# Optimization experiments

Hardware: AMD Instinct MI355X
Metric: run time of the kernel (lower is better)

The kernel has to match this reference:

```python
import jax, jax.numpy as jnp
import numpy as np
from jax import lax

RES = 64  # feature-map resolution after the stride-2 maxpool (input_size // 2)


def build_grid(res):
    # [1, res, res, 4]: (y, x, 1-y, 1-x) normalized coords, matching torch build_grid
    r = jnp.linspace(0.0, 1.0, res)
    yy, xx = jnp.meshgrid(r, r, indexing='ij')
    g = jnp.stack([yy, xx], axis=-1)[None]  # [1, res, res, 2]
    return jnp.concatenate([g, 1.0 - g], axis=-1)


def setup_inputs() -> dict:
    key = jax.random.key(0)
    ks = jax.random.split(key, 8)
    B, O, S = 8, 32, 128
    images = jax.random.normal(ks[0], (B, 12, S, S), dtype=jnp.float32)
    rois = jax.random.randint(ks[1], (B, O, S, S), 0, 2) > 0  # bool object masks
    gt_pos = jax.random.uniform(ks[2], (B, 4, O, 2), dtype=jnp.float32)
    conv1_w = jax.random.normal(ks[3], (64, 12, 7, 7), dtype=jnp.float32) * 0.05
    conv1_b = jnp.zeros((64,), dtype=jnp.float32)
    conv2_w = jax.random.normal(ks[4], (128, 64, 3, 3), dtype=jnp.float32) * 0.05
    conv2_b = jnp.zeros((128,), dtype=jnp.float32)
    pe_w = jax.random.normal(ks[5], (128, 4), dtype=jnp.float32) * 0.5
    pe_b = jnp.zeros((128,), dtype=jnp.float32)
    return {"images": images, "rois": rois, "gt_pos": gt_pos,
            "conv1_w": conv1_w, "conv1_b": conv1_b,
            "conv2_w": conv2_w, "conv2_b": conv2_b,
            "pe_w": pe_w, "pe_b": pe_b}


def _forward(images, rois, conv1_w, conv1_b, conv2_w, conv2_b, pe_w, pe_b):
    dn = ('NCHW', 'OIHW', 'NCHW')
    # conv1 7x7 pad 3 + ReLU
    x = lax.conv_general_dilated(images, conv1_w, (1, 1), [(3, 3), (3, 3)], dimension_numbers=dn)
    x = jax.nn.relu(x + conv1_b[None, :, None, None])
    # maxpool 2x2 stride 2
    x = lax.reduce_window(x, -jnp.inf, lax.max, (1, 1, 2, 2), (1, 1, 2, 2), 'VALID')
    # conv2 3x3 pad 1 + ReLU -> [B, 128, 64, 64]
    x = lax.conv_general_dilated(x, conv2_w, (1, 1), [(1, 1), (1, 1)], dimension_numbers=dn)
    x = jax.nn.relu(x + conv2_b[None, :, None, None])
    # soft position embedding: Linear(4->128) on grid, added per-pixel
    grid = build_grid(RES)  # [1, 64, 64, 4]
    emb = jnp.einsum('ihwf,cf->ichw', grid, pe_w) + pe_b[None, :, None, None]
    x = x + emb
    # roi_pool: nearest-downsample masks 128->64 (stride-2 gather matches torch nearest),
    # broadcast-multiply, then spatial max -> [B, O, C]
    m = rois[:, :, ::2, ::2].astype(x.dtype)  # [B, O, 64, 64]
    masked = x[:, None] * m[:, :, None]       # [B, O, C, 64, 64] (huge intermediate)
    return jnp.max(masked, axis=(-1, -2))


def reference(images, rois, gt_pos, conv1_w, conv1_b, conv2_w, conv2_b, pe_w, pe_b):
    # gt_pos is unused because use_ground_truth_pos=False
    return _forward(images, rois, conv1_w, conv1_b, conv2_w, conv2_b, pe_w, pe_b)
```

## Files before the change

kernel.cpp:

```cpp
#include <hip/hip_runtime.h>
#include <math.h>

typedef __attribute__((ext_vector_type(8))) short bf16x8;
typedef __attribute__((ext_vector_type(4))) float f32x4;
typedef __attribute__((ext_vector_type(8))) unsigned short ushort8;

#define N_IMT  (8*136*136*16)
#define N_PT   (8*66*66*64)
#define N_X2   (8*128*64*64)
#define N_PARTIAL (8*32*8*128)
#define N_WB1  (25*4*64*8)
#define N_WB2  (18*8*64*8)

__device__ inline unsigned short f2bf(float f) {
    unsigned u = __float_as_uint(f);
    u += 0x7FFF + ((u >> 16) & 1);
    return (unsigned short)(u >> 16);
}
__device__ inline float bf2f(unsigned short h) {
    return __uint_as_float(((unsigned)h) << 16);
}

__global__ void k_zero(unsigned* __restrict__ p, int n) {
    int stride = gridDim.x * 256;
    for (int i = blockIdx.x * 256 + threadIdx.x; i < n; i += stride) p[i] = 0u;
}

__global__ void k_prep(const float* __restrict__ images,
                       const float* __restrict__ w1, const float* __restrict__ w2,
                       unsigned short* __restrict__ imTh, unsigned short* __restrict__ imTl,
                       unsigned short* __restrict__ wB1h, unsigned short* __restrict__ wB1l,
                       unsigned short* __restrict__ wB2h, unsigned short* __restrict__ wB2l)
{
    const int bid = blockIdx.x, tid = threadIdx.x;
    if (bid < 512) {
        int t = bid * 256 + tid;
        int b = t >> 14, rem = t & 16383;
        int y = rem >> 7, x = rem & 127;
        ushort8 h0, h1, l0, l1;
        #pragma unroll
        for (int j = 0; j < 8; ++j) {
            float v = images[((b * 12 + j) << 14) + (y << 7) + x];
            unsigned short h = f2bf(v);
            h0[j] = h; l0[j] = f2bf(v - bf2f(h));
        }
        #pragma unroll
        for (int j = 0; j < 4; ++j) {
            float v = images[((b * 12 + 8 + j) << 14) + (y << 7) + x];
            unsigned short h = f2bf(v);
            h1[j] = h; l1[j] = f2bf(v - bf2f(h));
        }
        #pragma unroll
        for (int j = 4; j < 8; ++j) { h1[j] = 0; l1[j] = 0; }
        int base = ((b * 136 + y + 3) * 136 + x + 3) * 16;
        *(ushort8*)(imTh + base) = h0;  *(ushort8*)(imTh + base + 8) = h1;
        *(ushort8*)(imTl + base) = l0;  *(ushort8*)(imTl + base + 8) = l1;
    } else if (bid < 537) {
        int s = bid - 512;
        int n = tid >> 6, l = tid & 63;
        int oc = n * 16 + (l & 15), g = l >> 4;
        int tap = 2 * s + (g >> 1);
        ushort8 hi, lo;
        #pragma unroll
        for (int j = 0; j < 8; ++j) {
            int ic = (g & 1) * 8 + j;
            float v = (tap < 49 && ic < 12) ? w1[oc * 588 + ic * 49 + tap] : 0.0f;
            unsigned short h = f2bf(v);
            hi[j] = h; lo[j] = f2bf(v - bf2f(h));
        }
        int idx = ((s * 4 + n) * 64 + l) * 8;
        *(ushort8*)(wB1h + idx) = hi;  *(ushort8*)(wB1l + idx) = lo;
    } else {
        int u = bid - 537;
        int s = u >> 1, nh = u & 1;
        int n = nh * 4 + (tid >> 6), l = tid & 63;
        int oc = n * 16 + (l & 15);
        int tap = s >> 1;
        ushort8 hi, lo;
        #pragma unroll
        for (int j = 0; j < 8; ++j) {
            int ic = (s & 1) * 32 + (l >> 4) * 8 + j;
            float v = w2[oc * 576 + ic * 9 + tap];
            unsigned short h = f2bf(v);
            hi[j] = h; lo[j] = f2bf(v - bf2f(h));
        }
        int idx = ((s * 8 + n) * 64 + l) * 8;
        *(ushort8*)(wB2h + idx) = hi;  *(ushort8*)(wB2l + idx) = lo;
    }
}

__global__ __launch_bounds__(256, 4) void k1_mfma(
    const unsigned short* __restrict__ imTh, const unsigned short* __restrict__ imTl,
    const unsigned short* __restrict__ wB1h, const unsigned short* __restrict__ wB1l,
    const float* __restrict__ b1,
    unsigned short* __restrict__ pTh, unsigned short* __restrict__ pTl)
{
    const int bid = blockIdx.x;
    const int b  = bid & 7;
    const int rest = bid >> 3;
    const int y0 = rest & 63;
    const int x0 = (rest >> 6) * 64;
    const int tid = threadIdx.x;
    const int w  = __builtin_amdgcn_readfirstlane(tid >> 6);
    const int l  = tid & 63;
    const int px = l & 15;
    const int g  = l >> 4;
    const int gq = g >> 1;
    const int baseA = ((b * 136 + 2 * y0) * 136 + (x0 + w * 16 + px)) * 16 + (g & 1) * 8;

    f32x4 acc[2][4];
    #pragma unroll
    for (int m = 0; m < 2; ++m)
        #pragma unroll
        for (int n = 0; n < 4; ++n) acc[m][n] = (f32x4)(0.0f);

    #pragma unroll
    for (int s = 0; s < 25; ++s) {
        const int t0 = 2 * s, t1 = 2 * s + 1;
        const int off0 = ((t0 / 7) * 136 + (t0 % 7)) * 16;
        const int off1 = ((t1 / 7) * 136 + (t1 % 7)) * 16;
        int offA = gq ? off1 : off0;
        bf16x8 Ah0 = *(const bf16x8*)(imTh + baseA + offA);
        bf16x8 Ah1 = *(const bf16x8*)(imTh + baseA + 2176 + offA);
        bf16x8 Al0 = *(const bf16x8*)(imTl + baseA + offA);
        bf16x8 Al1 = *(const bf16x8*)(imTl + baseA + 2176 + offA);
        const unsigned short* wb = wB1h + s * 2048 + l * 8;
        const unsigned short* wl2 = wB1l + s * 2048 + l * 8;
        #pragma unroll
        for (int n = 0; n < 4; ++n) {
            bf16x8 Bh = *(const bf16x8*)(wb + n * 512);
            bf16x8 Bl = *(const bf16x8*)(wl2 + n * 512);
            acc[0][n] = __builtin_amdgcn_mfma_f32_16x16x32_bf16(Ah0, Bh, acc[0][n], 0, 0, 0);
            acc[0][n] = __builtin_amdgcn_mfma_f32_16x16x32_bf16(Ah0, Bl, acc[0][n], 0, 0, 0);
            acc[0][n] = __builtin_amdgcn_mfma_f32_16x16x32_bf16(Al0, Bh, acc[0][n], 0, 0, 0);
            acc[1][n] = __builtin_amdgcn_mfma_f32_16x16x32_bf16(Ah1, Bh, acc[1][n], 0, 0, 0);
            acc[1][n] = __builtin_amdgcn_mfma_f32_16x16x32_bf16(Ah1, Bl, acc[1][n], 0, 0, 0);
            acc[1][n] = __builtin_amdgcn_mfma_f32_16x16x32_bf16(Al1, Bh, acc[1][n], 0, 0, 0);
        }
    }

    #pragma unroll
    for (int n = 0; n < 4; ++n) {
        int oc = n * 16 + px;
        float bias = b1[oc];
        #pragma unroll
        for (int pp = 0; pp < 2; ++pp) {
            int e = pp * 2;
            float m = fmaxf(fmaxf(acc[0][n][e], acc[0][n][e + 1]),
                            fmaxf(acc[1][n][e], acc[1][n][e + 1]));
            float v = fmaxf(m + bias, 0.0f);
            unsigned short h = f2bf(v);
            unsigned short lo = f2bf(v - bf2f(h));
            int pcol = (x0 >> 1) + w * 8 + g * 2 + pp;
            int pidx = ((b * 66 + y0 + 1) * 66 + pcol + 1) * 64 + oc;
            pTh[pidx] = h; pTl[pidx] = lo;
        }
    }
}

__global__ __launch_bounds__(256, 4) void k2_mfma(
    const unsigned short* __restrict__ pTh, const unsigned short* __restrict__ pTl,
    const unsigned short* __restrict__ wB2h, const unsigned short* __restrict__ wB2l,
    const float* __restrict__ b2, const float* __restrict__ pew,
    const float* __restrict__ peb, float* __restrict__ x2)
{
    const int bid = blockIdx.x;
    const int b   = bid & 7;
    const int rest = bid >> 3;
    const int y   = rest & 63;
    const int ocg = rest >> 6;
    const int tid = threadIdx.x;
    const int w  = __builtin_amdgcn_readfirstlane(tid >> 6);
    const int l  = tid & 63;
    const int px = l & 15;
    const int g  = l >> 4;
    const int baseA = ((b * 66 + y) * 66 + (w * 16 + px)) * 64 + g * 8;

    f32x4 acc[4];
    #pragma unroll
    for (int n = 0; n < 4; ++n) acc[n] = (f32x4)(0.0f);

    #pragma unroll
    for (int s = 0; s < 18; ++s) {
        const int tap = s >> 1;
        const int offA = ((tap / 3) * 66 + (tap % 3)) * 64 + (s & 1) * 32;
        bf16x8 Ah = *(const bf16x8*)(pTh + baseA + offA);
        bf16x8 Al = *(const bf16x8*)(pTl + baseA + offA);
        const unsigned short* wb = wB2h + s * 4096 + (ocg * 4) * 512 + l * 8;
        const unsigned short* wl2 = wB2l + s * 4096 + (ocg * 4) * 512 + l * 8;
        #pragma unroll
        for (int n = 0; n < 4; ++n) {
            bf16x8 Bh = *(const bf16x8*)(wb + n * 512);
            bf16x8 Bl = *(const bf16x8*)(wl2 + n * 512);
            acc[n] = __builtin_amdgcn_mfma_f32_16x16x32_bf16(Ah, Bh, acc[n], 0, 0, 0);
            acc[n] = __builtin_amdgcn_mfma_f32_16x16x32_bf16(Ah, Bl, acc[n], 0, 0, 0);
            acc[n] = __builtin_amdgcn_mfma_f32_16x16x32_bf16(Al, Bh, acc[n], 0, 0, 0);
        }
    }

    const float inv63 = 1.0f / 63.0f;
    float yn = (float)y * inv63;
    #pragma unroll
    for (int n = 0; n < 4; ++n) {
        int oc = ocg * 64 + n * 16 + px;
        float bias = b2[oc];
        float e0 = pew[oc * 4 + 0], e1 = pew[oc * 4 + 1];
        float e2 = pew[oc * 4 + 2], e3 = pew[oc * 4 + 3];
        float rowc = peb[oc] + yn * e0 + (1.0f - yn) * e2;
        f32x4 st;
        #pragma unroll
        for (int e = 0; e < 4; ++e) {
            int x = w * 16 + g * 4 + e;
            float xn = (float)x * inv63;
            st[e] = fmaxf(acc[n][e] + bias, 0.0f) + rowc + xn * e1 + (1.0f - xn) * e3;
        }
        *(f32x4*)&x2[((b * 128 + oc) * 64 + y) * 64 + w * 16 + g * 4] = st;
    }
}

__global__ __launch_bounds__(256, 4) void k_roi(
    const float* __restrict__ x2, const int* __restrict__ rois,
    float* __restrict__ partial)
{
    __shared__ float mlds[16 * 512];
    const int tid = threadIdx.x;
    const int bid = blockIdx.x;
    const int b    = bid & 7;
    const int rest = bid >> 3;
    const int og   = rest & 1;
    const int pe   = (rest >> 1) & 7;
    const int cg   = rest >> 4;

    for (int idx = tid; idx < 16 * 512; idx += 256) {
        int ol = idx >> 9;
        int pp = idx & 511;
        int pxx = pe * 512 + pp;
        int h = pxx >> 6, ww = pxx & 63;
        mlds[idx] = rois[((b * 32 + og * 16 + ol) << 14) + (h << 8) + (ww << 1)] ? 1.0f : 0.0f;
    }
    __syncthreads();

    const int waveU = __builtin_amdgcn_readfirstlane(tid >> 6);
    const int lane  = tid & 63;
    const int c0    = cg * 16 + waveU * 4;

    float acc[4][16];
    #pragma unroll
    for (int c = 0; c < 4; ++c)
        #pragma unroll
        for (int o = 0; o < 16; ++o) acc[c][o] = -INFINITY;

    #pragma unroll 1
    for (int step = 0; step < 8; ++step) {
        int pp = step * 64 + lane;
        float m[16];
        #pragma unroll
        for (int o = 0; o < 16; ++o) m[o] = mlds[o * 512 + pp];
        const float* xb = &x2[(b * 128 + c0) * 4096 + pe * 512 + pp];
        #pragma unroll
        for (int c = 0; c < 4; ++c) {
            float x = xb[c * 4096];
            #pragma unroll
            for (int o = 0; o < 16; ++o)
                acc[c][o] = fmaxf(acc[c][o], x * m[o]);
        }
    }

    #pragma unroll
    for (int c = 0; c < 4; ++c)
        #pragma unroll
        for (int o = 0; o < 16; ++o) {
            float v = acc[c][o];
            #pragma unroll
            for (int mm = 1; mm < 64; mm <<= 1)
                v = fmaxf(v, __shfl_xor(v, mm, 64));
            if (lane == o * 4 + c)
                partial[((b * 32 + og * 16 + o) * 8 + pe) * 128 + c0 + c] = v;
        }
}

__global__ void k_reduce(const float* __restrict__ partial, float* __restrict__ out) {
    int idx = blockIdx.x * 256 + threadIdx.x;
    int c  = idx & 127;
    int bo = idx >> 7;
    float v = partial[bo * 8 * 128 + c];
    #pragma unroll
    for (int pe = 1; pe < 8; ++pe)
        v = fmaxf(v, partial[(bo * 8 + pe) * 128 + c]);
    out[idx] = v;
}

extern "C" void kernel_launch(void* const* d_in, const int* in_sizes, int n_in,
                              void* d_out, int out_size, void* d_ws, size_t ws_size,
                              hipStream_t stream) {
    const float* images = (const float*)d_in[0];
    const int*   rois   = (const int*)d_in[1];
    const float* w1  = (const float*)d_in[3];
    const float* b1  = (const float*)d_in[4];
    const float* w2  = (const float*)d_in[5];
    const float* b2  = (const float*)d_in[6];
    const float* pew = (const float*)d_in[7];
    const float* peb = (const float*)d_in[8];
    float* out = (float*)d_out;

    unsigned short* imTh = (unsigned short*)d_ws;
    unsigned short* imTl = imTh + N_IMT;
    unsigned short* pTh  = imTl + N_IMT;
    unsigned short* pTl  = pTh  + N_PT;
    float* x2      = (float*)(pTl + N_PT);
    float* partial = x2 + N_X2;
    unsigned short* wB1h = (unsigned short*)(partial + N_PARTIAL);
    unsigned short* wB1l = wB1h + N_WB1;
    unsigned short* wB2h = wB1l + N_WB1;
    unsigned short* wB2l = wB2h + N_WB2;

    const int nzero = (2 * N_IMT + 2 * N_PT) / 2;
    k_zero<<<2048, 256, 0, stream>>>((unsigned*)d_ws, nzero);
    k_prep<<<573, 256, 0, stream>>>(images, w1, w2, imTh, imTl, wB1h, wB1l, wB2h, wB2l);
    k1_mfma<<<1024, 256, 0, stream>>>(imTh, imTl, wB1h, wB1l, b1, pTh, pTl);
    k2_mfma<<<1024, 256, 0, stream>>>(pTh, pTl, wB2h, wB2l, b2, pew, peb, x2);
    k_roi<<<1024, 256, 0, stream>>>(x2, rois, partial);
    k_reduce<<<128, 256, 0, stream>>>(partial, out);
}
```

Baseline: 201.0 us.

## Double-buffer MFMA operand loads and widen conv2 tiles to two 16-pixel blocks

Both conv kernels now prefetch the next K-step's A and B operands into a second register set while issuing MFMAs on the current set, so global-load latency overlaps with matrix math. Conv2 also gives each wave two 16-pixel A tiles that share one set of B loads. This halves the conv2 grid and cuts redundant weight loads. The extra registers force launch bounds to drop from 4 to 3 waves per SIMD, which lowers occupancy.

```diff
diff --git a/kernel.cpp b/kernel.cpp
--- a/kernel.cpp
+++ b/kernel.cpp
@@ -89,7 +89,12 @@
     }
 }
 
-__global__ __launch_bounds__(256, 4) void k1_mfma(
+struct Ops {
+    bf16x8 Ah0, Ah1, Al0, Al1;
+    bf16x8 Bh0, Bh1, Bh2, Bh3, Bl0, Bl1, Bl2, Bl3;
+};
+
+__global__ __launch_bounds__(256, 3) void k1_mfma(
     const unsigned short* __restrict__ imTh, const unsigned short* __restrict__ imTl,
     const unsigned short* __restrict__ wB1h, const unsigned short* __restrict__ wB1l,
     const float* __restrict__ b1,
@@ -114,30 +119,47 @@
         #pragma unroll
         for (int n = 0; n < 4; ++n) acc[m][n] = (f32x4)(0.0f);
 
+#define K1_LOAD(O, s) { \
+    const int t0 = 2 * (s), t1 = 2 * (s) + 1; \
+    const int o0 = ((t0 / 7) * 136 + (t0 % 7)) * 16; \
+    const int o1 = ((t1 / 7) * 136 + (t1 % 7)) * 16; \
+    int offA = gq ? o1 : o0; \
+    O.Ah0 = *(const bf16x8*)(imTh + baseA + offA); \
+    O.Ah1 = *(const bf16x8*)(imTh + baseA + 2176 + offA); \
+    O.Al0 = *(const bf16x8*)(imTl + baseA + offA); \
+    O.Al1 = *(const bf16x8*)(imTl + baseA + 2176 + offA); \
+    const unsigned short* wb  = wB1h + (s) * 2048 + l * 8; \
+    const unsigned short* wl2 = wB1l + (s) * 2048 + l * 8; \
+    O.Bh0 = *(const bf16x8*)(wb);         O.Bh1 = *(const bf16x8*)(wb + 512); \
+    O.Bh2 = *(const bf16x8*)(wb + 1024);  O.Bh3 = *(const bf16x8*)(wb + 1536); \
+    O.Bl0 = *(const bf16x8*)(wl2);        O.Bl1 = *(const bf16x8*)(wl2 + 512); \
+    O.Bl2 = *(const bf16x8*)(wl2 + 1024); O.Bl3 = *(const bf16x8*)(wl2 + 1536); }
+
+#define K1_MFMA_N(O, n) \
+    acc[0][n] = __builtin_amdgcn_mfma_f32_16x16x32_bf16(O.Ah0, O.Bh##n, acc[0][n], 0, 0, 0); \
+    acc[0][n] = __builtin_amdgcn_mfma_f32_16x16x32_bf16(O.Ah0, O.Bl##n, acc[0][n], 0, 0, 0); \
+    acc[0][n] = __builtin_amdgcn_mfma_f32_16x16x32_bf16(O.Al0, O.Bh##n, acc[0][n], 0, 0, 0); \
+    acc[1][n] = __builtin_amdgcn_mfma_f32_16x16x32_bf16(O.Ah1, O.Bh##n, acc[1][n], 0, 0, 0); \
+    acc[1][n] = __builtin_amdgcn_mfma_f32_16x16x32_bf16(O.Ah1, O.Bl##n, acc[1][n], 0, 0, 0); \
+    acc[1][n] = __builtin_amdgcn_mfma_f32_16x16x32_bf16(O.Al1, O.Bh##n, acc[1][n], 0, 0, 0);
+
+#define K1_MFMA_ALL(O) { K1_MFMA_N(O, 0) K1_MFMA_N(O, 1) K1_MFMA_N(O, 2) K1_MFMA_N(O, 3) }
+
+    Ops oA, oB;
+    K1_LOAD(oA, 0)
     #pragma unroll
     for (int s = 0; s < 25; ++s) {
-        const int t0 = 2 * s, t1 = 2 * s + 1;
-        const int off0 = ((t0 / 7) * 136 + (t0 % 7)) * 16;
-        const int off1 = ((t1 / 7) * 136 + (t1 % 7)) * 16;
-        int offA = gq ? off1 : off0;
-        bf16x8 Ah0 = *(const bf16x8*)(imTh + baseA + offA);
-        bf16x8 Ah1 = *(const bf16x8*)(imTh + baseA + 2176 + offA);
-        bf16x8 Al0 = *(const bf16x8*)(imTl + baseA + offA);
-        bf16x8 Al1 = *(const bf16x8*)(imTl + baseA + 2176 + offA);
-        const unsigned short* wb = wB1h + s * 2048 + l * 8;
-        const unsigned short* wl2 = wB1l + s * 2048 + l * 8;
-        #pragma unroll
-        for (int n = 0; n < 4; ++n) {
-            bf16x8 Bh = *(const bf16x8*)(wb + n * 512);
-            bf16x8 Bl = *(const bf16x8*)(wl2 + n * 512);
-            acc[0][n] = __builtin_amdgcn_mfma_f32_16x16x32_bf16(Ah0, Bh, acc[0][n], 0, 0, 0);
-            acc[0][n] = __builtin_amdgcn_mfma_f32_16x16x32_bf16(Ah0, Bl, acc[0][n], 0, 0, 0);
-            acc[0][n] = __builtin_amdgcn_mfma_f32_16x16x32_bf16(Al0, Bh, acc[0][n], 0, 0, 0);
-            acc[1][n] = __builtin_amdgcn_mfma_f32_16x16x32_bf16(Ah1, Bh, acc[1][n], 0, 0, 0);
-            acc[1][n] = __builtin_amdgcn_mfma_f32_16x16x32_bf16(Ah1, Bl, acc[1][n], 0, 0, 0);
-            acc[1][n] = __builtin_amdgcn_mfma_f32_16x16x32_bf16(Al1, Bh, acc[1][n], 0, 0, 0);
-        }
-    }
+        if ((s & 1) == 0) {
+            if (s < 24) { K1_LOAD(oB, s + 1) }
+            K1_MFMA_ALL(oA)
+        } else {
+            if (s < 24) { K1_LOAD(oA, s + 1) }
+            K1_MFMA_ALL(oB)
+        }
+    }
+#undef K1_LOAD
+#undef K1_MFMA_N
+#undef K1_MFMA_ALL
 
     #pragma unroll
     for (int n = 0; n < 4; ++n) {
@@ -158,7 +180,7 @@
     }
 }
 
-__global__ __launch_bounds__(256, 4) void k2_mfma(
+__global__ __launch_bounds__(256, 3) void k2_mfma(
     const unsigned short* __restrict__ pTh, const unsigned short* __restrict__ pTl,
     const unsigned short* __restrict__ wB2h, const unsigned short* __restrict__ wB2l,
     const float* __restrict__ b2, const float* __restrict__ pew,
@@ -167,36 +189,62 @@
     const int bid = blockIdx.x;
     const int b   = bid & 7;
     const int rest = bid >> 3;
-    const int y   = rest & 63;
-    const int ocg = rest >> 6;
+    const int y2  = rest & 31;
+    const int ocg = rest >> 5;
     const int tid = threadIdx.x;
     const int w  = __builtin_amdgcn_readfirstlane(tid >> 6);
     const int l  = tid & 63;
     const int px = l & 15;
     const int g  = l >> 4;
-    const int baseA = ((b * 66 + y) * 66 + (w * 16 + px)) * 64 + g * 8;
-
-    f32x4 acc[4];
-    #pragma unroll
-    for (int n = 0; n < 4; ++n) acc[n] = (f32x4)(0.0f);
-
+    const int y     = y2 * 2 + (w >> 1);
+    const int xbase = (w & 1) * 32;
+    const int baseA = ((b * 66 + y) * 66 + (xbase + px)) * 64 + g * 8;
+
+    f32x4 acc[2][4];
+    #pragma unroll
+    for (int m = 0; m < 2; ++m)
+        #pragma unroll
+        for (int n = 0; n < 4; ++n) acc[m][n] = (f32x4)(0.0f);
+
+#define K2_LOAD(O, s) { \
+    const int tap = (s) >> 1; \
+    const int offA = ((tap / 3) * 66 + (tap % 3)) * 64 + ((s) & 1) * 32; \
+    O.Ah0 = *(const bf16x8*)(pTh + baseA + offA); \
+    O.Ah1 = *(const bf16x8*)(pTh + baseA + 1024 + offA); \
+    O.Al0 = *(const bf16x8*)(pTl + baseA + offA); \
+    O.Al1 = *(const bf16x8*)(pTl + baseA + 1024 + offA); \
+    const unsigned short* wb  = wB2h + (s) * 4096 + ocg * 2048 + l * 8; \
+    const unsigned short* wl2 = wB2l + (s) * 4096 + ocg * 2048 + l * 8; \
+    O.Bh0 = *(const bf16x8*)(wb);         O.Bh1 = *(const bf16x8*)(wb + 512); \
+    O.Bh2 = *(const bf16x8*)(wb + 1024);  O.Bh3 = *(const bf16x8*)(wb + 1536); \
+    O.Bl0 = *(const bf16x8*)(wl2);        O.Bl1 = *(const bf16x8*)(wl2 + 512); \
+    O.Bl2 = *(const bf16x8*)(wl2 + 1024); O.Bl3 = *(const bf16x8*)(wl2 + 1536); }
+
+#define K2_MFMA_N(O, n) \
+    acc[0][n] = __builtin_amdgcn_mfma_f32_16x16x32_bf16(O.Ah0, O.Bh##n, acc[0][n], 0, 0, 0); \
+    acc[0][n] = __builtin_amdgcn_mfma_f32_16x16x32_bf16(O.Ah0, O.Bl##n, acc[0][n], 0, 0, 0); \
+    acc[0][n] = __builtin_amdgcn_mfma_f32_16x16x32_bf16(O.Al0, O.Bh##n, acc[0][n], 0, 0, 0); \
+    acc[1][n] = __builtin_amdgcn_mfma_f32_16x16x32_bf16(O.Ah1, O.Bh##n, acc[1][n], 0, 0, 0); \
+    acc[1][n] = __builtin_amdgcn_mfma_f32_16x16x32_bf16(O.Ah1, O.Bl##n, acc[1][n], 0, 0, 0); \
+    acc[1][n] = __builtin_amdgcn_mfma_f32_16x16x32_bf16(O.Al1, O.Bh##n, acc[1][n], 0, 0, 0);
+
+#define K2_MFMA_ALL(O) { K2_MFMA_N(O, 0) K2_MFMA_N(O, 1) K2_MFMA_N(O, 2) K2_MFMA_N(O, 3) }
+
+    Ops oA, oB;
+    K2_LOAD(oA, 0)
     #pragma unroll
     for (int s = 0; s < 18; ++s) {
-        const int tap = s >> 1;
-        const int offA = ((tap / 3) * 66 + (tap % 3)) * 64 + (s & 1) * 32;
-        bf16x8 Ah = *(const bf16x8*)(pTh + baseA + offA);
-        bf16x8 Al = *(const bf16x8*)(pTl + baseA + offA);
-        const unsigned short* wb = wB2h + s * 4096 + (ocg * 4) * 512 + l * 8;
-        const unsigned short* wl2 = wB2l + s * 4096 + (ocg * 4) * 512 + l * 8;
-        #pragma unroll
-        for (int n = 0; n < 4; ++n) {
-            bf16x8 Bh = *(const bf16x8*)(wb + n * 512);
-            bf16x8 Bl = *(const bf16x8*)(wl2 + n * 512);
-            acc[n] = __builtin_amdgcn_mfma_f32_16x16x32_bf16(Ah, Bh, acc[n], 0, 0, 0);
-            acc[n] = __builtin_amdgcn_mfma_f32_16x16x32_bf16(Ah, Bl, acc[n], 0, 0, 0);
-            acc[n] = __builtin_amdgcn_mfma_f32_16x16x32_bf16(Al, Bh, acc[n], 0, 0, 0);
-        }
-    }
+        if ((s & 1) == 0) {
+            if (s < 17) { K2_LOAD(oB, s + 1) }
+            K2_MFMA_ALL(oA)
+        } else {
+            if (s < 17) { K2_LOAD(oA, s + 1) }
+            K2_MFMA_ALL(oB)
+        }
+    }
+#undef K2_LOAD
+#undef K2_MFMA_N
+#undef K2_MFMA_ALL
 
     const float inv63 = 1.0f / 63.0f;
     float yn = (float)y * inv63;
@@ -207,14 +255,17 @@
         float e0 = pew[oc * 4 + 0], e1 = pew[oc * 4 + 1];
         float e2 = pew[oc * 4 + 2], e3 = pew[oc * 4 + 3];
         float rowc = peb[oc] + yn * e0 + (1.0f - yn) * e2;
-        f32x4 st;
-        #pragma unroll
-        for (int e = 0; e < 4; ++e) {
-            int x = w * 16 + g * 4 + e;
-            float xn = (float)x * inv63;
-            st[e] = fmaxf(acc[n][e] + bias, 0.0f) + rowc + xn * e1 + (1.0f - xn) * e3;
-        }
-        *(f32x4*)&x2[((b * 128 + oc) * 64 + y) * 64 + w * 16 + g * 4] = st;
+        #pragma unroll
+        for (int mm = 0; mm < 2; ++mm) {
+            f32x4 st;
+            #pragma unroll
+            for (int e = 0; e < 4; ++e) {
+                int x = xbase + mm * 16 + g * 4 + e;
+                float xn = (float)x * inv63;
+                st[e] = fmaxf(acc[mm][n][e] + bias, 0.0f) + rowc + xn * e1 + (1.0f - xn) * e3;
+            }
+            *(f32x4*)&x2[((b * 128 + oc) * 64 + y) * 64 + xbase + mm * 16 + g * 4] = st;
+        }
     }
 }
 
@@ -318,7 +369,7 @@
     k_zero<<<2048, 256, 0, stream>>>((unsigned*)d_ws, nzero);
     k_prep<<<573, 256, 0, stream>>>(images, w1, w2, imTh, imTl, wB1h, wB1l, wB2h, wB2l);
     k1_mfma<<<1024, 256, 0, stream>>>(imTh, imTl, wB1h, wB1l, b1, pTh, pTl);
-    k2_mfma<<<1024, 256, 0, stream>>>(pTh, pTl, wB2h, wB2l, b2, pew, peb, x2);
+    k2_mfma<<<512, 256, 0, stream>>>(pTh, pTl, wB2h, wB2l, b2, pew, peb, x2);
     k_roi<<<1024, 256, 0, stream>>>(x2, rois, partial);
     k_reduce<<<128, 256, 0, stream>>>(partial, out);
 }
```

New measurement: 201.3 us. No clear change (+0.2%).
